# Kernel tuning notes

Hardware: AMD Instinct MI355X
Metric: run time of the kernel (lower is better)

Reference implementation:

```python
import jax, jax.numpy as jnp
import numpy as np

HIDDEN = 1024
N_HEAD = 16
N_KV_HEAD = 4
HEAD_DIM = HIDDEN // N_HEAD  # 64


def setup_inputs() -> dict:
    key = jax.random.key(0)
    ks = jax.random.split(key, 9)
    s = 0.02
    kv_dim = N_KV_HEAD * HEAD_DIM
    return {
        "X": jax.random.normal(ks[0], (2, 2048, HIDDEN), dtype=jnp.float32),
        "Wq": jax.random.normal(ks[1], (HIDDEN, HIDDEN), dtype=jnp.float32) * s,
        "bq": jnp.zeros((HIDDEN,), dtype=jnp.float32),
        "Wk": jax.random.normal(ks[2], (HIDDEN, kv_dim), dtype=jnp.float32) * s,
        "bk": jnp.zeros((kv_dim,), dtype=jnp.float32),
        "Wv": jax.random.normal(ks[3], (HIDDEN, kv_dim), dtype=jnp.float32) * s,
        "bv": jnp.zeros((kv_dim,), dtype=jnp.float32),
        "Wo": jax.random.normal(ks[4], (HIDDEN, HIDDEN), dtype=jnp.float32) * s,
        "bo": jnp.zeros((HIDDEN,), dtype=jnp.float32),
    }


def reference(X, Wq, bq, Wk, bk, Wv, bv, Wo, bo):
    B, S, _ = X.shape
    rep = N_HEAD // N_KV_HEAD
    # projections
    q = (X @ Wq + bq).reshape(B, S, N_HEAD, HEAD_DIM).transpose(0, 2, 1, 3)      # [B,H,S,D]
    k = (X @ Wk + bk).reshape(B, S, N_KV_HEAD, HEAD_DIM).transpose(0, 2, 1, 3)   # [B,Hkv,S,D]
    v = (X @ Wv + bv).reshape(B, S, N_KV_HEAD, HEAD_DIM).transpose(0, 2, 1, 3)
    # repeat_interleave KV heads to full head count (faithful to original)
    k = jnp.repeat(k, rep, axis=1)  # [B,H,S,D]
    v = jnp.repeat(v, rep, axis=1)
    scale = 1.0 / jnp.sqrt(jnp.float32(HEAD_DIM))
    scores = jnp.einsum("bhqd,bhkd->bhqk", q, k) * scale  # [B,H,S,S]
    weights = jax.nn.softmax(scores, axis=-1)
    out = jnp.einsum("bhqk,bhkd->bhqd", weights, v)       # [B,H,S,D]
    out = out.transpose(0, 2, 1, 3).reshape(B, S, HIDDEN)
    return out @ Wo + bo
```

## Files before the change

kernel.cpp:

```cpp
#include <hip/hip_runtime.h>
#include <hip/hip_bf16.h>

#define HIDDEN 1024
#define NHEAD 16
#define NKV 4
#define HDIM 64
#define KVDIM 256
#define SEQ 2048
#define BATCH 2
#define NQKV 1536

typedef __attribute__((ext_vector_type(4)))  float f32x4;
typedef __attribute__((ext_vector_type(16))) float f32x16;
typedef __attribute__((ext_vector_type(8)))  short s16x8;
typedef __attribute__((ext_vector_type(4)))  short s16x4;

#if defined(__has_builtin)
#if __has_builtin(__builtin_amdgcn_exp2f)
#define EXP2F(x) __builtin_amdgcn_exp2f(x)
#else
#define EXP2F(x) exp2f(x)
#endif
#else
#define EXP2F(x) exp2f(x)
#endif

static __device__ __forceinline__ ushort f2bf(float f) {
    union { __hip_bfloat16 b; ushort u; } cv; cv.b = __float2bfloat16(f); return cv.u;
}
static __device__ __forceinline__ unsigned cvtpk2_rhu(float a, float b) {
    float ah = __uint_as_float(__float_as_uint(a) + 0x8000u);
    float bh = __uint_as_float(__float_as_uint(b) + 0x8000u);
    unsigned r;
    asm("v_cvt_pk_bf16_f32 %0, %1, %2" : "=v"(r) : "v"(ah), "v"(bh));
    return r;
}
static __device__ __forceinline__ void plane32_swap(unsigned& a, unsigned& b) {
    asm("v_permlane32_swap_b32 %0, %1" : "+v"(a), "+v"(b));
}
static __device__ __forceinline__ void async16(const void* g, void* l) {
    __builtin_amdgcn_global_load_lds((__attribute__((address_space(1))) void*)g,
                                     (__attribute__((address_space(3))) void*)l, 16, 0, 0);
}

__global__ __launch_bounds__(256)
void prep(const float* __restrict__ X, ushort* __restrict__ Xb,
          const float* __restrict__ Wq, const float* __restrict__ Wk,
          const float* __restrict__ Wv, ushort* __restrict__ Tqkv,
          const float* __restrict__ Wo, ushort* __restrict__ Two)
{
    __shared__ float Tl[64][65];
    const int bid = blockIdx.x, tid = threadIdx.x;

    if (bid < 4096) {
        int i = bid * 256 + tid;
        float4 v = ((const float4*)X)[i];
        ushort4 o;
        o.x = f2bf(v.x); o.y = f2bf(v.y); o.z = f2bf(v.z); o.w = f2bf(v.w);
        ((ushort4*)Xb)[i] = o;
        return;
    }

    const float* W; ushort* T; int N, n0, k0, roff;
    if (bid < 4096 + 384) {
        int wq = bid - 4096;
        int bx = wq % 24; k0 = (wq / 24) * 64;
        T = Tqkv;
        if (bx < 16)      { W = Wq; N = 1024; n0 = bx * 64;        roff = 0; }
        else if (bx < 20) { W = Wk; N = 256;  n0 = (bx - 16) * 64; roff = 1024; }
        else              { W = Wv; N = 256;  n0 = (bx - 20) * 64; roff = 1280; }
    } else {
        int wo = bid - 4480;
        int bx = wo % 16; k0 = (wo / 16) * 64;
        W = Wo; T = Two; N = 1024; n0 = bx * 64; roff = 0;
    }

#pragma unroll
    for (int it = 0; it < 4; it++) {
        int idx = tid + it * 256;
        int kk = idx >> 4, n4 = (idx & 15) * 4;
        float4 v = *(const float4*)(W + (size_t)(k0 + kk) * N + n0 + n4);
        Tl[kk][n4 + 0] = v.x; Tl[kk][n4 + 1] = v.y;
        Tl[kk][n4 + 2] = v.z; Tl[kk][n4 + 3] = v.w;
    }
    __syncthreads();
#pragma unroll
    for (int it = 0; it < 4; it++) {
        int idx = tid + it * 256;
        int n = idx >> 4, k4 = (idx & 15) * 4;
        ushort4 h4;
        h4.x = f2bf(Tl[k4 + 0][n]); h4.y = f2bf(Tl[k4 + 1][n]);
        h4.z = f2bf(Tl[k4 + 2][n]); h4.w = f2bf(Tl[k4 + 3][n]);
        *(ushort4*)(T + (size_t)(roff + n0 + n) * HIDDEN + k0 + k4) = h4;
    }
}

template <int MODE>
__global__ __launch_bounds__(256)
void gemm_bf(const ushort* __restrict__ A, const ushort* __restrict__ Bt,
             const float* __restrict__ b0, const float* __restrict__ b1,
             const float* __restrict__ b2, void* __restrict__ Cout,
             int M, int N, int K)
{
    __shared__ __align__(16) ushort Ah[128 * 64];
    __shared__ __align__(16) ushort Bh[128 * 64];

    const int tid = threadIdx.x;
    const int lane = tid & 63, wv = tid >> 6;
    const int wr = wv >> 1, wc = wv & 1;
    const int m = lane & 15, c = lane >> 4;

    const int nwg = gridDim.x * gridDim.y;
    const int flat = blockIdx.y * gridDim.x + blockIdx.x;
    const int swz = (flat & 7) * (nwg >> 3) + (flat >> 3);
    const int bx = swz % gridDim.x, by = swz / gridDim.x;
    const int row0 = by * 128, col0 = bx * 128;

    const ushort* gA[4]; const ushort* gB[4]; int ldsO[4];
#pragma unroll
    for (int it = 0; it < 4; it++) {
        int idx = it * 256 + tid;
        gA[it] = A  + (size_t)(row0 + (idx >> 3)) * K + (idx & 7) * 8;
        gB[it] = Bt + (size_t)(col0 + (idx >> 3)) * K + (idx & 7) * 8;
        ldsO[it] = idx * 8;
    }

    f32x4 acc[4][4];
#pragma unroll
    for (int t = 0; t < 4; t++)
#pragma unroll
        for (int u = 0; u < 4; u++) acc[t][u] = (f32x4){0.f, 0.f, 0.f, 0.f};

    for (int k0 = 0; k0 < K; k0 += 64) {
        __syncthreads();
#pragma unroll
        for (int it = 0; it < 4; it++) {
            async16(gA[it] + k0, Ah + ldsO[it]);
            async16(gB[it] + k0, Bh + ldsO[it]);
        }
        __syncthreads();

#pragma unroll
        for (int kk = 0; kk < 2; kk++) {
            s16x8 ah[4], bh[4];
#pragma unroll
            for (int t = 0; t < 4; t++)
                ah[t] = *(const s16x8*)&Ah[(wr * 64 + t * 16 + m) * 64 + kk * 32 + c * 8];
#pragma unroll
            for (int u = 0; u < 4; u++)
                bh[u] = *(const s16x8*)&Bh[(wc * 64 + u * 16 + m) * 64 + kk * 32 + c * 8];
#pragma unroll
            for (int t = 0; t < 4; t++)
#pragma unroll
                for (int u = 0; u < 4; u++)
                    acc[t][u] = __builtin_amdgcn_mfma_f32_16x16x32_bf16(ah[t], bh[u], acc[t][u], 0, 0, 0);
        }
    }

    const int orow = row0 + wr * 64 + 4 * c;
    const int ocol = col0 + wc * 64 + m;
    if (MODE == 0) {
        ushort* Cb = (ushort*)Cout;
#pragma unroll
        for (int u = 0; u < 4; u++) {
            int n = ocol + 16 * u;
            float bias, scl;
            if (n < 1024)      { bias = b0[n];        scl = 0.18033688f; }
            else if (n < 1280) { bias = b1[n - 1024]; scl = 1.0f; }
            else               { bias = b2[n - 1280]; scl = 1.0f; }
#pragma unroll
            for (int t = 0; t < 4; t++)
#pragma unroll
                for (int r = 0; r < 4; r++)
                    Cb[(size_t)(orow + 16 * t + r) * N + n] = f2bf((acc[t][u][r] + bias) * scl);
        }
    } else {
        float* Cf = (float*)Cout;
#pragma unroll
        for (int u = 0; u < 4; u++) {
            int n = ocol + 16 * u;
            float bias = b0[n];
#pragma unroll
            for (int t = 0; t < 4; t++)
#pragma unroll
                for (int r = 0; r < 4; r++)
                    Cf[(size_t)(orow + 16 * t + r) * N + n] = acc[t][u][r] + bias;
        }
    }
}

__global__ __launch_bounds__(256)
void kvpack(const ushort* __restrict__ QKV, ushort* __restrict__ Kf,
            ushort* __restrict__ Vf)
{
    __shared__ __align__(16) ushort Kt[64][72];
    __shared__ __align__(16) ushort Vt[64][72];
    const int kt = blockIdx.x, hk = blockIdx.y, b = blockIdx.z;
    const int tid = threadIdx.x;

#pragma unroll
    for (int it = 0; it < 2; it++) {
        int idx = tid + it * 256;
        int r = idx >> 3, c8 = (idx & 7) * 8;
        const ushort* src = QKV + (size_t)(b * SEQ + kt * 64 + r) * NQKV + hk * HDIM + c8;
        *(s16x8*)&Kt[r][c8] = *(const s16x8*)(src + 1024);
        *(s16x8*)&Vt[r][c8] = *(const s16x8*)(src + 1280);
    }
    __syncthreads();

#pragma unroll
    for (int it = 0; it < 2; it++) {
        int idx = tid + it * 256;
        int t32 = idx >> 8, kc = (idx >> 6) & 3, lane = idx & 63;
        int n32 = lane & 31, h5 = lane >> 5;
        s16x8 fr = *(const s16x8*)&Kt[t32 * 32 + n32][kc * 16 + h5 * 8];
        size_t flat = ((size_t)(((b * NKV + hk) * 64 + kt * 2 + t32) * 4 + kc) * 64 + lane) * 8;
        *(s16x8*)(Kf + flat) = fr;
    }
#pragma unroll
    for (int it = 0; it < 2; it++) {
        int idx = tid + it * 256;
        int kcdn = idx >> 6, lane = idx & 63;
        int kc = kcdn >> 1, dn = kcdn & 1;
        int n32 = lane & 31, h5 = lane >> 5;
        s16x8 fr;
#pragma unroll
        for (int j = 0; j < 8; j++)
            fr[j] = (short)Vt[kc * 16 + h5 * 8 + j][dn * 32 + n32];
        size_t flat = ((size_t)(((b * NKV + hk) * 32 + kt) * 8 + kc * 2 + dn) * 64 + lane) * 8;
        *(s16x8*)(Vf + flat) = fr;
    }
}

__global__ __launch_bounds__(512, 2)
void attn_mfma14(const ushort* __restrict__ QKV, const ushort* __restrict__ Kf,
                 const ushort* __restrict__ Vf, ushort* __restrict__ Chi)
{
    __shared__ float OLb[4 * 32 * 64];
    __shared__ float LLb[4 * 32];

    const int tid = threadIdx.x, w = tid >> 6, lane = tid & 63;
    const int g = w >> 2, ws_ = w & 3;
    const int n32 = lane & 31, h5 = lane >> 5;
    const int h = blockIdx.y, b = blockIdx.z, hk = h >> 2;
    const int q0 = blockIdx.x * 64 + g * 32;

    const ushort* qrow = QKV + (size_t)(b * SEQ + q0 + n32) * NQKV + h * HDIM + h5 * 8;
    s16x8 aq[4];
#pragma unroll
    for (int kc = 0; kc < 4; kc++) aq[kc] = *(const s16x8*)(qrow + kc * 16);

    f32x16 accO[2];
#pragma unroll
    for (int j = 0; j < 16; j++) { accO[0][j] = 0.f; accO[1][j] = 0.f; }
    float lsum = 0.f;

    const ushort* kf0 = Kf + (size_t)(b * NKV + hk) * (64 * 4 * 64 * 8) + (size_t)lane * 8;
    const ushort* vf0 = Vf + (size_t)(b * NKV + hk) * (32 * 8 * 64 * 8) + (size_t)lane * 8;

    s16x8 kreg[8], vreg[8], pa[4];

#define LOAD_K(kt_) do {                                                      \
    _Pragma("unroll")                                                         \
    for (int kn = 0; kn < 2; kn++)                                            \
        _Pragma("unroll")                                                     \
        for (int kc = 0; kc < 4; kc++)                                        \
            kreg[kn * 4 + kc] =                                               \
                *(const s16x8*)(kf0 + (size_t)(((kt_) * 2 + kn) * 4 + kc) * 512); \
} while (0)

#define LOAD_V(kt_) do {                                                      \
    _Pragma("unroll")                                                         \
    for (int kc = 0; kc < 4; kc++)                                            \
        _Pragma("unroll")                                                     \
        for (int dn = 0; dn < 2; dn++)                                        \
            vreg[kc * 2 + dn] =                                               \
                *(const s16x8*)(vf0 + (size_t)((kt_) * 8 + kc * 2 + dn) * 512); \
} while (0)

#define QK_EXP_PACK() do {                                                    \
    _Pragma("unroll")                                                         \
    for (int kn = 0; kn < 2; kn++) {                                          \
        f32x16 S;                                                             \
        _Pragma("unroll")                                                     \
        for (int j = 0; j < 16; j++) S[j] = 0.f;                              \
        _Pragma("unroll")                                                     \
        for (int kc = 0; kc < 4; kc++)                                        \
            S = __builtin_amdgcn_mfma_f32_32x32x16_bf16(kreg[kn * 4 + kc],    \
                    aq[kc], S, 0, 0, 0);                                      \
        float p[16];                                                          \
        _Pragma("unroll")                                                     \
        for (int reg = 0; reg < 16; reg++) p[reg] = EXP2F(S[reg]);            \
        {                                                                     \
            float a0 = p[0] + p[1],   a1 = p[2] + p[3];                       \
            float a2 = p[4] + p[5],   a3 = p[6] + p[7];                       \
            float a4 = p[8] + p[9],   a5 = p[10] + p[11];                     \
            float a6 = p[12] + p[13], a7 = p[14] + p[15];                     \
            lsum += ((a0 + a1) + (a2 + a3)) + ((a4 + a5) + (a6 + a7));        \
        }                                                                     \
        {                                                                     \
            unsigned w0 = cvtpk2_rhu(p[0],  p[1]);                 \
            unsigned w1 = cvtpk2_rhu(p[2],  p[3]);                 \
            unsigned w2 = cvtpk2_rhu(p[4],  p[5]);                 \
            unsigned w3 = cvtpk2_rhu(p[6],  p[7]);                 \
            plane32_swap(w0, w2); plane32_swap(w1, w3);                       \
            union { s16x8 v; unsigned u[4]; } P0;                             \
            P0.u[0] = w0; P0.u[1] = w1; P0.u[2] = w2; P0.u[3] = w3;           \
            pa[kn * 2 + 0] = P0.v;                                            \
            unsigned w4 = cvtpk2_rhu(p[8],  p[9]);                 \
            unsigned w5 = cvtpk2_rhu(p[10], p[11]);                \
            unsigned w6 = cvtpk2_rhu(p[12], p[13]);                \
            unsigned w7 = cvtpk2_rhu(p[14], p[15]);                \
            plane32_swap(w4, w6); plane32_swap(w5, w7);                       \
            union { s16x8 v; unsigned u[4]; } P1;                             \
            P1.u[0] = w4; P1.u[1] = w5; P1.u[2] = w6; P1.u[3] = w7;           \
            pa[kn * 2 + 1] = P1.v;                                            \
        }                                                                     \
    }                                                                         \
} while (0)

#define PV_STEP() do {                                                        \
    _Pragma("unroll")                                                         \
    for (int kc = 0; kc < 4; kc++) {                                          \
        _Pragma("unroll")                                                     \
        for (int dn = 0; dn < 2; dn++)                                        \
            accO[dn] = __builtin_amdgcn_mfma_f32_32x32x16_bf16(pa[kc],        \
                           vreg[kc * 2 + dn], accO[dn], 0, 0, 0);             \
    }                                                                         \
} while (0)

    LOAD_K(ws_);
    LOAD_V(ws_);
    QK_EXP_PACK();
    LOAD_K(ws_ + 4);

#pragma unroll
    for (int i = 1; i < 8; i++) {
        PV_STEP();
        LOAD_V(ws_ + 4 * i);
        QK_EXP_PACK();
        if (i < 7) LOAD_K(ws_ + 4 * (i + 1));
    }
    PV_STEP();

#undef LOAD_K
#undef LOAD_V
#undef QK_EXP_PACK
#undef PV_STEP

    lsum += __shfl_xor(lsum, 32, 64);

    const int qq = tid >> 4;
    const int d0 = (tid & 15) * 4;
#pragma unroll
    for (int phase = 0; phase < 2; phase++) {
        if (g == phase) {
#pragma unroll
            for (int reg = 0; reg < 16; reg++) {
                int q = (reg & 3) + 8 * (reg >> 2) + 4 * h5;
                OLb[(ws_ * 32 + q) * 64 + n32]      = accO[0][reg];
                OLb[(ws_ * 32 + q) * 64 + 32 + n32] = accO[1][reg];
            }
            if (h5 == 0) LLb[ws_ * 32 + n32] = lsum;
        }
        __syncthreads();
        {
            float lsum2 = LLb[qq] + LLb[32 + qq] + LLb[64 + qq] + LLb[96 + qq];
            float inv = 1.f / lsum2;
            ushort4 hs;
            float o0 = (OLb[(0 * 32 + qq) * 64 + d0 + 0] + OLb[(1 * 32 + qq) * 64 + d0 + 0] +
                        OLb[(2 * 32 + qq) * 64 + d0 + 0] + OLb[(3 * 32 + qq) * 64 + d0 + 0]) * inv;
            float o1 = (OLb[(0 * 32 + qq) * 64 + d0 + 1] + OLb[(1 * 32 + qq) * 64 + d0 + 1] +
                        OLb[(2 * 32 + qq) * 64 + d0 + 1] + OLb[(3 * 32 + qq) * 64 + d0 + 1]) * inv;
            float o2 = (OLb[(0 * 32 + qq) * 64 + d0 + 2] + OLb[(1 * 32 + qq) * 64 + d0 + 2] +
                        OLb[(2 * 32 + qq) * 64 + d0 + 2] + OLb[(3 * 32 + qq) * 64 + d0 + 2]) * inv;
            float o3 = (OLb[(0 * 32 + qq) * 64 + d0 + 3] + OLb[(1 * 32 + qq) * 64 + d0 + 3] +
                        OLb[(2 * 32 + qq) * 64 + d0 + 3] + OLb[(3 * 32 + qq) * 64 + d0 + 3]) * inv;
            hs.x = f2bf(o0); hs.y = f2bf(o1); hs.z = f2bf(o2); hs.w = f2bf(o3);
            size_t off = (size_t)(b * SEQ + blockIdx.x * 64 + phase * 32 + qq) * HIDDEN
                       + h * HDIM + d0;
            *(ushort4*)(Chi + off) = hs;
        }
        __syncthreads();
    }
}

extern "C" void kernel_launch(void* const* d_in, const int* in_sizes, int n_in,
                              void* d_out, int out_size, void* d_ws, size_t ws_size,
                              hipStream_t stream)
{
    const float* X  = (const float*)d_in[0];
    const float* Wq = (const float*)d_in[1];
    const float* bq = (const float*)d_in[2];
    const float* Wk = (const float*)d_in[3];
    const float* bk = (const float*)d_in[4];
    const float* Wv = (const float*)d_in[5];
    const float* bv = (const float*)d_in[6];
    const float* Wo = (const float*)d_in[7];
    const float* bo = (const float*)d_in[8];
    float* out = (float*)d_out;

    const int M = BATCH * SEQ;
    char* ws = (char*)d_ws;
    ushort* Xb    = (ushort*)(ws);
    ushort* Ctx   = (ushort*)(ws + (8u  << 20));
    ushort* QKVb  = (ushort*)(ws + (16u << 20));
    ushort* Wqkvt = (ushort*)(ws + (28u << 20));
    ushort* Wot   = (ushort*)(ws + (31u << 20));
    ushort* Kf    = (ushort*)(ws + (33u << 20));
    ushort* Vf    = (ushort*)(ws + (35u << 20));

    prep<<<dim3(4736), 256, 0, stream>>>(X, Xb, Wq, Wk, Wv, Wqkvt, Wo, Wot);

    gemm_bf<0><<<dim3(NQKV / 128, M / 128), 256, 0, stream>>>(
        Xb, Wqkvt, bq, bk, bv, (void*)QKVb, M, NQKV, HIDDEN);

    kvpack<<<dim3(SEQ / 64, NKV, BATCH), 256, 0, stream>>>(QKVb, Kf, Vf);

    attn_mfma14<<<dim3(SEQ / 64, NHEAD, BATCH), 512, 0, stream>>>(QKVb, Kf, Vf, Ctx);

    gemm_bf<1><<<dim3(HIDDEN / 128, M / 128), 256, 0, stream>>>(
        Ctx, Wot, bo, nullptr, nullptr, (void*)out, M, HIDDEN, HIDDEN);
}
```

Before: 191.0 us.

## Fuse K/V fragment packing into QKV GEMM epilogue and drop kvpack kernel

```diff
diff --git a/kernel.cpp b/kernel.cpp
--- a/kernel.cpp
+++ b/kernel.cpp
@@ -100,10 +100,12 @@
 void gemm_bf(const ushort* __restrict__ A, const ushort* __restrict__ Bt,
              const float* __restrict__ b0, const float* __restrict__ b1,
              const float* __restrict__ b2, void* __restrict__ Cout,
+             ushort* __restrict__ Kf, ushort* __restrict__ Vf,
              int M, int N, int K)
 {
-    __shared__ __align__(16) ushort Ah[128 * 64];
-    __shared__ __align__(16) ushort Bh[128 * 64];
+    __shared__ __align__(16) ushort smem[17408];
+    ushort* Ah = smem;
+    ushort* Bh = smem + 128 * 64;
 
     const int tid = threadIdx.x;
     const int lane = tid & 63, wv = tid >> 6;
@@ -159,23 +161,66 @@
 
     const int orow = row0 + wr * 64 + 4 * c;
     const int ocol = col0 + wc * 64 + m;
+
+    if (MODE == 0 && bx >= 8) {
+        __syncthreads();
+#pragma unroll
+        for (int u = 0; u < 4; u++) {
+            int nloc = wc * 64 + m + 16 * u;
+            int gn = col0 + nloc;
+            float bias = (bx < 10) ? b1[gn - 1024] : b2[gn - 1280];
+#pragma unroll
+            for (int t = 0; t < 4; t++)
+#pragma unroll
+                for (int r = 0; r < 4; r++)
+                    smem[(wr * 64 + 4 * c + 16 * t + r) * 136 + nloc] =
+                        f2bf(acc[t][u][r] + bias);
+        }
+        __syncthreads();
+
+        const int b_  = row0 >> 11;
+        const int kt0 = (row0 & 2047) >> 6;
+        const int hk_base = (bx & 1) * 2;
+
+        if (bx < 10) {
+#pragma unroll
+            for (int it = 0; it < 8; it++) {
+                int idx = it * 256 + tid;
+                int lane_ = idx & 63, grp = idx >> 6;
+                int kc = grp & 3, t32 = (grp >> 2) & 1;
+                int ktt = (grp >> 3) & 1, hh = (grp >> 4) & 1;
+                int n32_ = lane_ & 31, h5_ = lane_ >> 5;
+                s16x8 fr = *(const s16x8*)&smem[(ktt * 64 + t32 * 32 + n32_) * 136
+                                                + hh * 64 + kc * 16 + h5_ * 8];
+                int hk = hk_base + hh, kt = kt0 + ktt;
+                size_t flatK = ((size_t)(((b_ * NKV + hk) * 64 + kt * 2 + t32) * 4 + kc) * 64
+                                + lane_) * 8;
+                *(s16x8*)(Kf + flatK) = fr;
+            }
+        } else {
+#pragma unroll
+            for (int it = 0; it < 8; it++) {
+                int idx = it * 256 + tid;
+                int lane_ = idx & 63, grp = idx >> 6;
+                int dn = grp & 1, kc = (grp >> 1) & 3;
+                int ktt = (grp >> 3) & 1, hh = (grp >> 4) & 1;
+                int n32_ = lane_ & 31, h5_ = lane_ >> 5;
+                s16x8 fr;
+#pragma unroll
+                for (int j = 0; j < 8; j++)
+                    fr[j] = (short)smem[(ktt * 64 + kc * 16 + h5_ * 8 + j) * 136
+                                        + hh * 64 + dn * 32 + n32_];
+                int hk = hk_base + hh, kt = kt0 + ktt;
+                size_t flatV = ((size_t)(((b_ * NKV + hk) * 32 + kt) * 8 + kc * 2 + dn) * 64
+                                + lane_) * 8;
+                *(s16x8*)(Vf + flatV) = fr;
+            }
+        }
+        return;
+    }
+
     if (MODE == 0) {
         ushort* Cb = (ushort*)Cout;
-#pragma unroll
-        for (int u = 0; u < 4; u++) {
-            int n = ocol + 16 * u;
-            float bias, scl;
-            if (n < 1024)      { bias = b0[n];        scl = 0.18033688f; }
-            else if (n < 1280) { bias = b1[n - 1024]; scl = 1.0f; }
-            else               { bias = b2[n - 1280]; scl = 1.0f; }
-#pragma unroll
-            for (int t = 0; t < 4; t++)
-#pragma unroll
-                for (int r = 0; r < 4; r++)
-                    Cb[(size_t)(orow + 16 * t + r) * N + n] = f2bf((acc[t][u][r] + bias) * scl);
-        }
-    } else {
-        float* Cf = (float*)Cout;
 #pragma unroll
         for (int u = 0; u < 4; u++) {
             int n = ocol + 16 * u;
@@ -184,51 +229,21 @@
             for (int t = 0; t < 4; t++)
 #pragma unroll
                 for (int r = 0; r < 4; r++)
+                    Cb[(size_t)(orow + 16 * t + r) * N + n] =
+                        f2bf((acc[t][u][r] + bias) * 0.18033688f);
+        }
+    } else {
+        float* Cf = (float*)Cout;
+#pragma unroll
+        for (int u = 0; u < 4; u++) {
+            int n = ocol + 16 * u;
+            float bias = b0[n];
+#pragma unroll
+            for (int t = 0; t < 4; t++)
+#pragma unroll
+                for (int r = 0; r < 4; r++)
                     Cf[(size_t)(orow + 16 * t + r) * N + n] = acc[t][u][r] + bias;
         }
-    }
-}
-
-__global__ __launch_bounds__(256)
-void kvpack(const ushort* __restrict__ QKV, ushort* __restrict__ Kf,
-            ushort* __restrict__ Vf)
-{
-    __shared__ __align__(16) ushort Kt[64][72];
-    __shared__ __align__(16) ushort Vt[64][72];
-    const int kt = blockIdx.x, hk = blockIdx.y, b = blockIdx.z;
-    const int tid = threadIdx.x;
-
-#pragma unroll
-    for (int it = 0; it < 2; it++) {
-        int idx = tid + it * 256;
-        int r = idx >> 3, c8 = (idx & 7) * 8;
-        const ushort* src = QKV + (size_t)(b * SEQ + kt * 64 + r) * NQKV + hk * HDIM + c8;
-        *(s16x8*)&Kt[r][c8] = *(const s16x8*)(src + 1024);
-        *(s16x8*)&Vt[r][c8] = *(const s16x8*)(src + 1280);
-    }
-    __syncthreads();
-
-#pragma unroll
-    for (int it = 0; it < 2; it++) {
-        int idx = tid + it * 256;
-        int t32 = idx >> 8, kc = (idx >> 6) & 3, lane = idx & 63;
-        int n32 = lane & 31, h5 = lane >> 5;
-        s16x8 fr = *(const s16x8*)&Kt[t32 * 32 + n32][kc * 16 + h5 * 8];
-        size_t flat = ((size_t)(((b * NKV + hk) * 64 + kt * 2 + t32) * 4 + kc) * 64 + lane) * 8;
-        *(s16x8*)(Kf + flat) = fr;
-    }
-#pragma unroll
-    for (int it = 0; it < 2; it++) {
-        int idx = tid + it * 256;
-        int kcdn = idx >> 6, lane = idx & 63;
-        int kc = kcdn >> 1, dn = kcdn & 1;
-        int n32 = lane & 31, h5 = lane >> 5;
-        s16x8 fr;
-#pragma unroll
-        for (int j = 0; j < 8; j++)
-            fr[j] = (short)Vt[kc * 16 + h5 * 8 + j][dn * 32 + n32];
-        size_t flat = ((size_t)(((b * NKV + hk) * 32 + kt) * 8 + kc * 2 + dn) * 64 + lane) * 8;
-        *(s16x8*)(Vf + flat) = fr;
     }
 }
 
@@ -413,12 +428,11 @@
     prep<<<dim3(4736), 256, 0, stream>>>(X, Xb, Wq, Wk, Wv, Wqkvt, Wo, Wot);
 
     gemm_bf<0><<<dim3(NQKV / 128, M / 128), 256, 0, stream>>>(
-        Xb, Wqkvt, bq, bk, bv, (void*)QKVb, M, NQKV, HIDDEN);
-
-    kvpack<<<dim3(SEQ / 64, NKV, BATCH), 256, 0, stream>>>(QKVb, Kf, Vf);
+        Xb, Wqkvt, bq, bk, bv, (void*)QKVb, Kf, Vf, M, NQKV, HIDDEN);
 
     attn_mfma14<<<dim3(SEQ / 64, NHEAD, BATCH), 512, 0, stream>>>(QKVb, Kf, Vf, Ctx);
 
     gemm_bf<1><<<dim3(HIDDEN / 128, M / 128), 256, 0, stream>>>(
-        Ctx, Wot, bo, nullptr, nullptr, (void*)out, M, HIDDEN, HIDDEN);
-}
+        Ctx, Wot, bo, nullptr, nullptr, (void*)out, nullptr, nullptr,
+        M, HIDDEN, HIDDEN);
+}
```

Measured after the change: 186.6 us. -2.3%, faster.
